# Kernel tuning notes

Hardware: AMD Instinct MI355X
Metric: run time of the kernel (lower is better)

The kernel has to match this reference:

```python
import jax, jax.numpy as jnp
import numpy as np

DIM_CODES = 512
DICT_SIZE = 512
EMBED_DIM = 16
BATCH = 512


def setup_inputs() -> dict:
    key = jax.random.key(0)
    k1, k2 = jax.random.split(key)
    mu = jax.random.normal(k1, (BATCH, DIM_CODES * EMBED_DIM), dtype=jnp.float32)
    dictionary = jax.random.normal(k2, (DIM_CODES, DICT_SIZE, EMBED_DIM), dtype=jnp.float32)
    return {"mu": mu, "dictionary": dictionary}


def reference(mu, dictionary):
    # mu: [B, C*E], dictionary: [C, K, E]
    B = mu.shape[0]
    C, K, E = dictionary.shape
    mu3 = mu.reshape(B, C, E)
    # pairwise squared distance ||mu - d||^2 = ||mu||^2 + ||d||^2 - 2 mu.d -> [B, C, K]
    dist = (jnp.sum(mu3 * mu3, axis=-1)[..., None]
            + jnp.sum(dictionary * dictionary, axis=-1)[None]
            - 2.0 * jnp.einsum('bce,cke->bck', mu3, dictionary))
    idx = jnp.argmin(dist, axis=-1)  # [B, C] int
    # gather nearest codebook entries: per-code index into its own codebook
    z_embed = dictionary[jnp.arange(C)[None, :], idx]  # [B, C, E]
    z_embed = z_embed.reshape(B, C * E)
    # TransferGrad: forward = z_embed, backward passes grad straight-through to mu
    z = mu + jax.lax.stop_gradient(z_embed - mu)
    one_hot_idx = jax.nn.one_hot(idx, K, dtype=mu.dtype)  # [B, C, K]
    return z, z_embed, one_hot_idx
```

## Files before the change

kernel.cpp:

```cpp
#include <hip/hip_runtime.h>
#include <float.h>

constexpr int C    = 512;
constexpr int K    = 512;
constexpr int E    = 16;
constexpr int B    = 512;
constexpr int ROWS = 128;
constexpr int MUS  = C * E;

__device__ __forceinline__ float fdot4(const float4 a, const float4 b, float acc) {
    acc = fmaf(a.x, b.x, acc);
    acc = fmaf(a.y, b.y, acc);
    acc = fmaf(a.z, b.z, acc);
    acc = fmaf(a.w, b.w, acc);
    return acc;
}
__device__ __forceinline__ double ddot4(const float4 a, const float4 b, double acc) {
    return acc + ((double)a.x * b.x + (double)a.y * b.y
                + (double)a.z * b.z + (double)a.w * b.w);
}
__device__ __forceinline__ double dnrm4(const float4 a, double acc) {
    return acc + ((double)a.x * a.x + (double)a.y * a.y
                + (double)a.z * a.z + (double)a.w * a.w);
}

__launch_bounds__(256, 1)
__global__ void vq_kernel(const float* __restrict__ mu,
                          const float* __restrict__ dict,
                          float* __restrict__ z,
                          float* __restrict__ zq,
                          float* __restrict__ oh)
{
    const int c    = blockIdx.x;
    const int b0   = blockIdx.y * ROWS;
    const int tid  = threadIdx.x;
    const int lane = tid & 63;
    const int wave = tid >> 6;

    __shared__ float mu_s[ROWS][E];

    const float* __restrict__ dbase = dict + (size_t)c * K * E;

#define FOR8(X) X(0) X(1) X(2) X(3) X(4) X(5) X(6) X(7)

#define DECL_D(i) float4 d##i##_0, d##i##_1, d##i##_2, d##i##_3; float n##i;
    FOR8(DECL_D)
#undef DECL_D

#define LOAD_D(i) { \
    const float4* p = reinterpret_cast<const float4*>( \
        dbase + (size_t)(lane + 64 * i) * E); \
    d##i##_0 = p[0]; d##i##_1 = p[1]; d##i##_2 = p[2]; d##i##_3 = p[3]; \
    float s = fdot4(d##i##_0, d##i##_0, 0.0f); \
    s = fdot4(d##i##_1, d##i##_1, s); \
    s = fdot4(d##i##_2, d##i##_2, s); \
    s = fdot4(d##i##_3, d##i##_3, s); \
    n##i = s; }
    FOR8(LOAD_D)
#undef LOAD_D

    {
        const int r = tid >> 2, q = tid & 3;
#pragma unroll
        for (int rep = 0; rep < 2; ++rep) {
            const int row = r + rep * 64;
            const float4* p = reinterpret_cast<const float4*>(
                mu + (size_t)(b0 + row) * MUS + c * E);
            reinterpret_cast<float4*>(&mu_s[row][0])[q] = p[q];
        }
    }
    __syncthreads();

#pragma unroll 1
    for (int j = 0; j < ROWS / 16; ++j) {
        unsigned long long pk0, pk1, pk2, pk3;
        float sec0, sec1, sec2, sec3;

#define DIST1(i) { \
    float acc = fdot4(d##i##_0, m0, 0.0f); \
    acc = fdot4(d##i##_1, m1, acc); \
    acc = fdot4(d##i##_2, m2, acc); \
    acc = fdot4(d##i##_3, m3, acc); \
    const float dist = fmaf(-2.0f, acc, nmu + n##i); \
    sc = fminf(sc, fmaxf(best_d, dist)); \
    if (dist < best_d) { best_d = dist; best_k = lane + 64 * i; } }

#define PHASE1(r) { \
    const int bl = wave + 16 * j + 4 * r; \
    const float4* mp = reinterpret_cast<const float4*>(&mu_s[bl][0]); \
    const float4 m0 = mp[0], m1 = mp[1], m2 = mp[2], m3 = mp[3]; \
    float nmu = fdot4(m0, m0, 0.0f); \
    nmu = fdot4(m1, m1, nmu); \
    nmu = fdot4(m2, m2, nmu); \
    nmu = fdot4(m3, m3, nmu); \
    float best_d = FLT_MAX; \
    int   best_k = K; \
    float sc     = FLT_MAX; \
    FOR8(DIST1) \
    pk##r = ((unsigned long long)__float_as_uint(best_d) << 32) \
          | (unsigned)best_k; \
    sec##r = sc; }

        PHASE1(0) PHASE1(1) PHASE1(2) PHASE1(3)
#undef PHASE1
#undef DIST1

#pragma unroll
        for (int off = 32; off; off >>= 1) {
#define SHUF(r) { \
            const unsigned long long o  = __shfl_down(pk##r, off); \
            const float              os = __shfl_down(sec##r, off); \
            const float ax = __uint_as_float((unsigned)(pk##r >> 32)); \
            const float bx = __uint_as_float((unsigned)(o     >> 32)); \
            sec##r = fminf(fminf(sec##r, os), fmaxf(ax, bx)); \
            if (o < pk##r) pk##r = o; }
            SHUF(0) SHUF(1) SHUF(2) SHUF(3)
#undef SHUF
        }

        int bk0, bk1, bk2, bk3;

#define D641(i) { \
    double nd = dnrm4(d##i##_0, 0.0); nd = dnrm4(d##i##_1, nd); \
    nd = dnrm4(d##i##_2, nd); nd = dnrm4(d##i##_3, nd); \
    double dt = ddot4(d##i##_0, m0, 0.0); dt = ddot4(d##i##_1, m1, dt); \
    dt = ddot4(d##i##_2, m2, dt); dt = ddot4(d##i##_3, m3, dt); \
    const double dist = nmuD + nd - 2.0 * dt; \
    if (dist < bdd) { bdd = dist; bkk = lane + 64 * i; } }

#define PHASE3(r, BK) { \
    const int klo = __builtin_amdgcn_readfirstlane((int)(unsigned)pk##r); \
    const int dhi = __builtin_amdgcn_readfirstlane((int)(pk##r >> 32)); \
    const int shi = __builtin_amdgcn_readfirstlane(__float_as_int(sec##r)); \
    int bkr = klo; \
    if (__int_as_float(shi) - __int_as_float(dhi) < 1e-3f) { \
         \
        const int bl = wave + 16 * j + 4 * r; \
        const float4* mp = reinterpret_cast<const float4*>(&mu_s[bl][0]); \
        const float4 m0 = mp[0], m1 = mp[1], m2 = mp[2], m3 = mp[3]; \
        double nmuD = dnrm4(m0, 0.0); nmuD = dnrm4(m1, nmuD); \
        nmuD = dnrm4(m2, nmuD); nmuD = dnrm4(m3, nmuD); \
        double bdd = DBL_MAX; \
        int    bkk = K; \
        FOR8(D641) \
        _Pragma("unroll") \
        for (int off = 32; off; off >>= 1) { \
            const double od = __shfl_down(bdd, off); \
            const int    ok = __shfl_down(bkk, off); \
            if (od < bdd || (od == bdd && ok < bkk)) { bdd = od; bkk = ok; } \
        } \
        bkr = __builtin_amdgcn_readfirstlane(bkk); \
    } \
    BK = bkr; \
    { \
        const int bl = wave + 16 * j + 4 * r; \
        float* ohp = oh + ((size_t)(b0 + bl) * C + c) * K; \
        _Pragma("unroll") \
        for (int h = 0; h < 2; ++h) { \
            const int kb = h * 256 + lane * 4; \
            float4 v; \
            v.x = (kb + 0 == bkr) ? 1.0f : 0.0f; \
            v.y = (kb + 1 == bkr) ? 1.0f : 0.0f; \
            v.z = (kb + 2 == bkr) ? 1.0f : 0.0f; \
            v.w = (kb + 3 == bkr) ? 1.0f : 0.0f; \
            *reinterpret_cast<float4*>(ohp + kb) = v; \
        } \
    } }

        PHASE3(0, bk0) PHASE3(1, bk1) PHASE3(2, bk2) PHASE3(3, bk3)
#undef PHASE3
#undef D641

        {
            const int r = lane >> 4;
            const int e = lane & 15;
            int bkr = bk0;
            bkr = (r == 1) ? bk1 : bkr;
            bkr = (r == 2) ? bk2 : bkr;
            bkr = (r == 3) ? bk3 : bkr;
            const int bl = wave + 16 * j + 4 * r;
            const float dq = dbase[bkr * E + e];
            const float mm = mu_s[bl][e];
            const size_t o = (size_t)(b0 + bl) * MUS + (size_t)c * E + e;
            zq[o] = dq;
            z[o]  = mm + (dq - mm);
        }
    }
#undef FOR8
}

extern "C" void kernel_launch(void* const* d_in, const int* in_sizes, int n_in,
                              void* d_out, int out_size, void* d_ws, size_t ws_size,
                              hipStream_t stream)
{
    const float* mu   = (const float*)d_in[0];
    const float* dict = (const float*)d_in[1];

    float* z  = (float*)d_out;
    float* zq = z  + (size_t)B * C * E;
    float* oh = zq + (size_t)B * C * E;

    dim3 grid(C, B / ROWS);
    vq_kernel<<<grid, 256, 0, stream>>>(mu, dict, z, zq, oh);
}
```

Measured before the change: 781.9 us.

## Map one batch row per thread and zero-fill one-hot before scattering ones

Restructures the work mapping so each thread owns one batch row and scans all 512 codes serially. Codebook entries are read via wave-uniform loads and code norms are precomputed into LDS. This replaces the cross-lane shuffle reductions with per-thread argmin and drops the constant ||mu||^2 term. The one-hot output is written as a bulk zero fill followed by a single scattered 1.0 store, ordered by a waitcnt. Occupancy hints are raised to 4 blocks per CU. The risks are that the fp64 fallback now runs serially per thread, causing divergence, and that correctness depends on the zero fill landing before the scattered ones, which come from other threads in the same wave.

After: 860.6 us. +10.1%, slower.

```diff
diff --git a/kernel.cpp b/kernel.cpp
--- a/kernel.cpp
+++ b/kernel.cpp
@@ -1,12 +1,12 @@
 #include <hip/hip_runtime.h>
 #include <float.h>
 
-constexpr int C    = 512;
-constexpr int K    = 512;
-constexpr int E    = 16;
-constexpr int B    = 512;
-constexpr int ROWS = 128;
-constexpr int MUS  = C * E;
+constexpr int C   = 512;
+constexpr int K   = 512;
+constexpr int E   = 16;
+constexpr int B   = 512;
+constexpr int RPB = 256;
+constexpr int MUS = C * E;
 
 __device__ __forceinline__ float fdot4(const float4 a, const float4 b, float acc) {
     acc = fmaf(a.x, b.x, acc);
@@ -24,7 +24,7 @@
                 + (double)a.z * a.z + (double)a.w * a.w);
 }
 
-__launch_bounds__(256, 1)
+__launch_bounds__(256, 4)
 __global__ void vq_kernel(const float* __restrict__ mu,
                           const float* __restrict__ dict,
                           float* __restrict__ z,
@@ -32,161 +32,100 @@
                           float* __restrict__ oh)
 {
     const int c    = blockIdx.x;
-    const int b0   = blockIdx.y * ROWS;
     const int tid  = threadIdx.x;
     const int lane = tid & 63;
-    const int wave = tid >> 6;
+    const int b    = blockIdx.y * RPB + tid;
 
-    __shared__ float mu_s[ROWS][E];
+    __shared__ float nd_s[K];
 
     const float* __restrict__ dbase = dict + (size_t)c * K * E;
 
-#define FOR8(X) X(0) X(1) X(2) X(3) X(4) X(5) X(6) X(7)
+    const float4* mp = reinterpret_cast<const float4*>(mu + (size_t)b * MUS + c * E);
+    const float4 m0 = mp[0], m1 = mp[1], m2 = mp[2], m3 = mp[3];
 
-#define DECL_D(i) float4 d##i##_0, d##i##_1, d##i##_2, d##i##_3; float n##i;
-    FOR8(DECL_D)
-#undef DECL_D
-
-#define LOAD_D(i) { \
-    const float4* p = reinterpret_cast<const float4*>( \
-        dbase + (size_t)(lane + 64 * i) * E); \
-    d##i##_0 = p[0]; d##i##_1 = p[1]; d##i##_2 = p[2]; d##i##_3 = p[3]; \
-    float s = fdot4(d##i##_0, d##i##_0, 0.0f); \
-    s = fdot4(d##i##_1, d##i##_1, s); \
-    s = fdot4(d##i##_2, d##i##_2, s); \
-    s = fdot4(d##i##_3, d##i##_3, s); \
-    n##i = s; }
-    FOR8(LOAD_D)
-#undef LOAD_D
+#pragma unroll
+    for (int rep = 0; rep < 2; ++rep) {
+        const int k = tid + rep * 256;
+        const float4* p = reinterpret_cast<const float4*>(dbase + (size_t)k * E);
+        const float4 a0 = p[0], a1 = p[1], a2 = p[2], a3 = p[3];
+        float s = fdot4(a0, a0, 0.0f);
+        s = fdot4(a1, a1, s);
+        s = fdot4(a2, a2, s);
+        s = fdot4(a3, a3, s);
+        nd_s[k] = s;
+    }
 
     {
-        const int r = tid >> 2, q = tid & 3;
-#pragma unroll
-        for (int rep = 0; rep < 2; ++rep) {
-            const int row = r + rep * 64;
-            const float4* p = reinterpret_cast<const float4*>(
-                mu + (size_t)(b0 + row) * MUS + c * E);
-            reinterpret_cast<float4*>(&mu_s[row][0])[q] = p[q];
+        const size_t rowstride = (size_t)C * K / 4;
+        float4* p = reinterpret_cast<float4*>(
+            oh + ((size_t)(blockIdx.y * RPB + (tid & ~63)) * C + c) * K) + lane;
+        const float4 z4 = make_float4(0.f, 0.f, 0.f, 0.f);
+#pragma unroll 4
+        for (int r = 0; r < 64; ++r) {
+            p[0]  = z4;
+            p[64] = z4;
+            p += rowstride;
         }
     }
+
     __syncthreads();
 
+    float best = FLT_MAX, sec = FLT_MAX;
+    int   bk   = 0;
 #pragma unroll 1
-    for (int j = 0; j < ROWS / 16; ++j) {
-        unsigned long long pk0, pk1, pk2, pk3;
-        float sec0, sec1, sec2, sec3;
+    for (int k4 = 0; k4 < K; k4 += 4) {
+        const float4 nd4 = *reinterpret_cast<const float4*>(&nd_s[k4]);
+#define CODE(J, ND) { \
+        const float4* p = reinterpret_cast<const float4*>( \
+            dbase + (size_t)(k4 + J) * E); \
+        const float4 a0 = p[0], a1 = p[1], a2 = p[2], a3 = p[3]; \
+        float dot = fdot4(a0, m0, 0.0f); \
+        dot = fdot4(a1, m1, dot); \
+        dot = fdot4(a2, m2, dot); \
+        dot = fdot4(a3, m3, dot); \
+        const float dist = fmaf(-2.0f, dot, ND); \
+        sec = fminf(sec, fmaxf(best, dist)); \
+        if (dist < best) { best = dist; bk = k4 + J; } }
+        CODE(0, nd4.x) CODE(1, nd4.y) CODE(2, nd4.z) CODE(3, nd4.w)
+#undef CODE
+    }
 
-#define DIST1(i) { \
-    float acc = fdot4(d##i##_0, m0, 0.0f); \
-    acc = fdot4(d##i##_1, m1, acc); \
-    acc = fdot4(d##i##_2, m2, acc); \
-    acc = fdot4(d##i##_3, m3, acc); \
-    const float dist = fmaf(-2.0f, acc, nmu + n##i); \
-    sc = fminf(sc, fmaxf(best_d, dist)); \
-    if (dist < best_d) { best_d = dist; best_k = lane + 64 * i; } }
+    if (sec - best < 2.5e-4f) {
+        double bdd = DBL_MAX;
+        int    bkk = 0;
+        for (int k = 0; k < K; ++k) {
+            const float4* p = reinterpret_cast<const float4*>(dbase + (size_t)k * E);
+            const float4 a0 = p[0], a1 = p[1], a2 = p[2], a3 = p[3];
+            double nd = dnrm4(a0, 0.0);
+            nd = dnrm4(a1, nd); nd = dnrm4(a2, nd); nd = dnrm4(a3, nd);
+            double dt = ddot4(a0, m0, 0.0);
+            dt = ddot4(a1, m1, dt); dt = ddot4(a2, m2, dt); dt = ddot4(a3, m3, dt);
+            const double dist = nd - 2.0 * dt;
+            if (dist < bdd) { bdd = dist; bkk = k; }
+        }
+        bk = bkk;
+    }
 
-#define PHASE1(r) { \
-    const int bl = wave + 16 * j + 4 * r; \
-    const float4* mp = reinterpret_cast<const float4*>(&mu_s[bl][0]); \
-    const float4 m0 = mp[0], m1 = mp[1], m2 = mp[2], m3 = mp[3]; \
-    float nmu = fdot4(m0, m0, 0.0f); \
-    nmu = fdot4(m1, m1, nmu); \
-    nmu = fdot4(m2, m2, nmu); \
-    nmu = fdot4(m3, m3, nmu); \
-    float best_d = FLT_MAX; \
-    int   best_k = K; \
-    float sc     = FLT_MAX; \
-    FOR8(DIST1) \
-    pk##r = ((unsigned long long)__float_as_uint(best_d) << 32) \
-          | (unsigned)best_k; \
-    sec##r = sc; }
+    {
+        const float4* qp = reinterpret_cast<const float4*>(dbase + (size_t)bk * E);
+        const float4 q0 = qp[0], q1 = qp[1], q2 = qp[2], q3 = qp[3];
+        float4* zo  = reinterpret_cast<float4*>(z  + (size_t)b * MUS + c * E);
+        float4* zqo = reinterpret_cast<float4*>(zq + (size_t)b * MUS + c * E);
+        zqo[0] = q0; zqo[1] = q1; zqo[2] = q2; zqo[3] = q3;
+        float4 r0, r1, r2, r3;
+        r0.x = m0.x + (q0.x - m0.x); r0.y = m0.y + (q0.y - m0.y);
+        r0.z = m0.z + (q0.z - m0.z); r0.w = m0.w + (q0.w - m0.w);
+        r1.x = m1.x + (q1.x - m1.x); r1.y = m1.y + (q1.y - m1.y);
+        r1.z = m1.z + (q1.z - m1.z); r1.w = m1.w + (q1.w - m1.w);
+        r2.x = m2.x + (q2.x - m2.x); r2.y = m2.y + (q2.y - m2.y);
+        r2.z = m2.z + (q2.z - m2.z); r2.w = m2.w + (q2.w - m2.w);
+        r3.x = m3.x + (q3.x - m3.x); r3.y = m3.y + (q3.y - m3.y);
+        r3.z = m3.z + (q3.z - m3.z); r3.w = m3.w + (q3.w - m3.w);
+        zo[0] = r0; zo[1] = r1; zo[2] = r2; zo[3] = r3;
+    }
 
-        PHASE1(0) PHASE1(1) PHASE1(2) PHASE1(3)
-#undef PHASE1
-#undef DIST1
-
-#pragma unroll
-        for (int off = 32; off; off >>= 1) {
-#define SHUF(r) { \
-            const unsigned long long o  = __shfl_down(pk##r, off); \
-            const float              os = __shfl_down(sec##r, off); \
-            const float ax = __uint_as_float((unsigned)(pk##r >> 32)); \
-            const float bx = __uint_as_float((unsigned)(o     >> 32)); \
-            sec##r = fminf(fminf(sec##r, os), fmaxf(ax, bx)); \
-            if (o < pk##r) pk##r = o; }
-            SHUF(0) SHUF(1) SHUF(2) SHUF(3)
-#undef SHUF
-        }
-
-        int bk0, bk1, bk2, bk3;
-
-#define D641(i) { \
-    double nd = dnrm4(d##i##_0, 0.0); nd = dnrm4(d##i##_1, nd); \
-    nd = dnrm4(d##i##_2, nd); nd = dnrm4(d##i##_3, nd); \
-    double dt = ddot4(d##i##_0, m0, 0.0); dt = ddot4(d##i##_1, m1, dt); \
-    dt = ddot4(d##i##_2, m2, dt); dt = ddot4(d##i##_3, m3, dt); \
-    const double dist = nmuD + nd - 2.0 * dt; \
-    if (dist < bdd) { bdd = dist; bkk = lane + 64 * i; } }
-
-#define PHASE3(r, BK) { \
-    const int klo = __builtin_amdgcn_readfirstlane((int)(unsigned)pk##r); \
-    const int dhi = __builtin_amdgcn_readfirstlane((int)(pk##r >> 32)); \
-    const int shi = __builtin_amdgcn_readfirstlane(__float_as_int(sec##r)); \
-    int bkr = klo; \
-    if (__int_as_float(shi) - __int_as_float(dhi) < 1e-3f) { \
-         \
-        const int bl = wave + 16 * j + 4 * r; \
-        const float4* mp = reinterpret_cast<const float4*>(&mu_s[bl][0]); \
-        const float4 m0 = mp[0], m1 = mp[1], m2 = mp[2], m3 = mp[3]; \
-        double nmuD = dnrm4(m0, 0.0); nmuD = dnrm4(m1, nmuD); \
-        nmuD = dnrm4(m2, nmuD); nmuD = dnrm4(m3, nmuD); \
-        double bdd = DBL_MAX; \
-        int    bkk = K; \
-        FOR8(D641) \
-        _Pragma("unroll") \
-        for (int off = 32; off; off >>= 1) { \
-            const double od = __shfl_down(bdd, off); \
-            const int    ok = __shfl_down(bkk, off); \
-            if (od < bdd || (od == bdd && ok < bkk)) { bdd = od; bkk = ok; } \
-        } \
-        bkr = __builtin_amdgcn_readfirstlane(bkk); \
-    } \
-    BK = bkr; \
-    { \
-        const int bl = wave + 16 * j + 4 * r; \
-        float* ohp = oh + ((size_t)(b0 + bl) * C + c) * K; \
-        _Pragma("unroll") \
-        for (int h = 0; h < 2; ++h) { \
-            const int kb = h * 256 + lane * 4; \
-            float4 v; \
-            v.x = (kb + 0 == bkr) ? 1.0f : 0.0f; \
-            v.y = (kb + 1 == bkr) ? 1.0f : 0.0f; \
-            v.z = (kb + 2 == bkr) ? 1.0f : 0.0f; \
-            v.w = (kb + 3 == bkr) ? 1.0f : 0.0f; \
-            *reinterpret_cast<float4*>(ohp + kb) = v; \
-        } \
-    } }
-
-        PHASE3(0, bk0) PHASE3(1, bk1) PHASE3(2, bk2) PHASE3(3, bk3)
-#undef PHASE3
-#undef D641
-
-        {
-            const int r = lane >> 4;
-            const int e = lane & 15;
-            int bkr = bk0;
-            bkr = (r == 1) ? bk1 : bkr;
-            bkr = (r == 2) ? bk2 : bkr;
-            bkr = (r == 3) ? bk3 : bkr;
-            const int bl = wave + 16 * j + 4 * r;
-            const float dq = dbase[bkr * E + e];
-            const float mm = mu_s[bl][e];
-            const size_t o = (size_t)(b0 + bl) * MUS + (size_t)c * E + e;
-            zq[o] = dq;
-            z[o]  = mm + (dq - mm);
-        }
-    }
-#undef FOR8
+    asm volatile("s_waitcnt vmcnt(0)" ::: "memory");
+    oh[((size_t)b * C + c) * K + bk] = 1.0f;
 }
 
 extern "C" void kernel_launch(void* const* d_in, const int* in_sizes, int n_in,
@@ -200,6 +139,6 @@
     float* zq = z  + (size_t)B * C * E;
     float* oh = zq + (size_t)B * C * E;
 
-    dim3 grid(C, B / ROWS);
+    dim3 grid(C, B / RPB);
     vq_kernel<<<grid, 256, 0, stream>>>(mu, dict, z, zq, oh);
 }
```
